# Performance work log

Measured on AMD Instinct MI355X. Metric: run time of the kernel, lower is better.

The kernel has to match this reference:

```python
import jax, jax.numpy as jnp
import numpy as np

N_NODES = 100_000
N_EDGES = 1_600_000
N_GRAPHS = 64
EPS = 1e-7  # GENConv message epsilon
D_IN, D_H, D_OUT, OUT_DIM = 128, 192, 128, 10


def _w(k, fan_in, fan_out):
    return jax.random.normal(k, (fan_in, fan_out), jnp.float32) * (1.0 / np.sqrt(fan_in))


def setup_inputs() -> dict:
    key = jax.random.key(0)
    ks = jax.random.split(key, 8)
    return {
        "x": jax.random.normal(ks[0], (N_NODES, D_IN), jnp.float32),
        "W0": _w(ks[1], D_IN, D_H), "b0": jnp.zeros((D_H,), jnp.float32),
        "W1": _w(ks[2], D_H, D_H), "b1": jnp.zeros((D_H,), jnp.float32),
        "W2": _w(ks[3], D_H, D_H), "b2": jnp.zeros((D_H,), jnp.float32),
        "W3": _w(ks[4], D_H, D_OUT), "b3": jnp.zeros((D_OUT,), jnp.float32),
        "Wfc": _w(ks[5], D_OUT, OUT_DIM), "bfc": jnp.zeros((OUT_DIM,), jnp.float32),
        "edge_index": jax.random.randint(ks[6], (2, N_EDGES), 0, N_NODES, jnp.int32),
        "batch": jnp.sort(jax.random.randint(ks[7], (N_NODES,), 0, N_GRAPHS, jnp.int32)),
    }


def _genconv(x, W, b, src, dst):
    # GENConv (num_layers=1, aggr='add'): message = relu(x_j) + eps,
    # scatter-add to dst, residual add, single Linear MLP.
    msg = jax.nn.relu(x[src]) + EPS          # [E, d]
    agg = jax.ops.segment_sum(msg, dst, num_segments=N_NODES)  # [N, d]
    return (x + agg) @ W + b


def reference(x, W0, b0, W1, b1, W2, b2, W3, b3, Wfc, bfc, edge_index, batch):
    src, dst = edge_index[0], edge_index[1]  # source_to_target flow
    for W, b in ((W0, b0), (W1, b1), (W2, b2), (W3, b3)):
        x = _genconv(x, W, b, src, dst)
    # global mean pool over graphs
    sums = jax.ops.segment_sum(x, batch, num_segments=N_GRAPHS)
    counts = jax.ops.segment_sum(jnp.ones((x.shape[0],), x.dtype), batch,
                                 num_segments=N_GRAPHS)
    pooled = sums / jnp.maximum(counts, 1.0)[:, None]  # [G, D_OUT]
    logits = pooled @ Wfc + bfc                        # [G, OUT_DIM]
    return jax.nn.log_softmax(logits, axis=1)
```

## Files before the change

kernel.cpp:

```cpp
#include <hip/hip_runtime.h>
#include <hip/hip_bf16.h>
#include <stdint.h>

constexpr int NN = 100000;
constexpr int NE = 1600000;
constexpr int NG = 64;
constexpr int S  = 192;
constexpr int NB_SCAN = 98;
constexpr int NN8 = 100352;
constexpr unsigned int ZOFF = (unsigned int)NN * 384u;

constexpr int PREP_INDEG_BLK = 1563;
constexpr int PREP_CONVX_BLK = 12500;
constexpr int PREP_CONVW_BLK = 384;
constexpr int PREP_GB_BLK    = 391;
constexpr int PREP_GRID = PREP_INDEG_BLK + PREP_CONVX_BLK + PREP_CONVW_BLK + PREP_GB_BLK;

constexpr int EG_BLOCKS = 391;
constexpr int HROW = 50048;
constexpr int SROW = HROW / 8;

typedef __bf16 bf16x8 __attribute__((ext_vector_type(8)));
typedef float  f32x16 __attribute__((ext_vector_type(16)));
typedef float  f32x2  __attribute__((ext_vector_type(2)));

union U16x4 { uint4 u; bf16x8 b; };

__device__ __forceinline__ float bl(unsigned int u) { return __uint_as_float(u << 16); }
__device__ __forceinline__ float bh(unsigned int u) { return __uint_as_float(u & 0xffff0000u); }
__device__ __forceinline__ float b16f(unsigned short u) { return __uint_as_float(((unsigned int)u) << 16); }
__device__ __forceinline__ unsigned int fb(float f) {
    unsigned int u = __float_as_uint(f);
    return (u + 0x7fffu + ((u >> 16) & 1u)) >> 16;
}
__device__ __forceinline__ unsigned int prelu(unsigned int u) {
    unsigned int r;
    asm("v_pk_max_f16 %0, %1, %2" : "=v"(r) : "v"(u), "v"(0u));
    return r;
}
__device__ __forceinline__ unsigned int cnt2bf(unsigned int h) {
    float f0 = (float)(h & 0xffffu);
    float f1 = (float)(h >> 16);
    return (__float_as_uint(f0) >> 16) | (__float_as_uint(f1) & 0xffff0000u);
}

__global__ __launch_bounds__(256) void k_prep(const float* __restrict__ x,
                                              const int* __restrict__ ei,
                                              const int* __restrict__ bat,
                                              const float* __restrict__ W0, const float* __restrict__ W1,
                                              const float* __restrict__ W2,
                                              unsigned short* __restrict__ A_,
                                              int* __restrict__ indeg8, int* __restrict__ slot,
                                              unsigned short* __restrict__ T0, unsigned short* __restrict__ T1,
                                              unsigned short* __restrict__ T2,
                                              int* __restrict__ nstart) {
    const int b = blockIdx.x;
    if (b < PREP_INDEG_BLK) {
        int e4 = (b * 256 + threadIdx.x) * 4;
        if (e4 < NE) {
            int* cp = indeg8 + (b & 7) * NN8;
            int4 d = *(const int4*)(ei + NE + e4);
            int4 sl;
            sl.x = atomicAdd(&cp[d.x], 1);
            sl.y = atomicAdd(&cp[d.y], 1);
            sl.z = atomicAdd(&cp[d.z], 1);
            sl.w = atomicAdd(&cp[d.w], 1);
            *(int4*)(slot + e4) = sl;
        }
    } else if (b < PREP_INDEG_BLK + PREP_CONVX_BLK) {
        int id = (b - PREP_INDEG_BLK) * 256 + threadIdx.x;
        if (id < 96) ((unsigned int*)(A_ + (size_t)NN * S))[id] = 0u;
        int row = id >> 5, c4 = id & 31;
        float4 v = ((const float4*)x)[id];
        uint2 a;
        a.x = fb(v.x) | (fb(v.y) << 16);
        a.y = fb(v.z) | (fb(v.w) << 16);
        *(uint2*)(A_ + row * S + c4 * 4) = a;
    } else if (b < PREP_INDEG_BLK + PREP_CONVX_BLK + PREP_CONVW_BLK) {
        int id = (b - PREP_INDEG_BLK - PREP_CONVX_BLK) * 256 + threadIdx.x;
        const float* W; unsigned short* T; int N, base;
        if      (id < 24576) { W = W0; T = T0; N = 192; base = 0;     }
        else if (id < 61440) { W = W1; T = T1; N = 192; base = 24576; }
        else                 { W = W2; T = T2; N = 192; base = 61440; }
        int lid = id - base;
        int ci = lid >> 3, j = lid & 7;
        int kc = ci / N, n = ci % N;
        T[lid] = (unsigned short)fb(W[(kc * 8 + j) * N + n]);
    } else {
        int n = (b - PREP_INDEG_BLK - PREP_CONVX_BLK - PREP_CONVW_BLK) * 256 + threadIdx.x;
        if (n < NN) {
            int b0 = bat[n];
            int bprev = (n == 0) ? -1 : bat[n - 1];
            for (int g = bprev + 1; g <= b0; g++) nstart[g] = n;
            if (n == NN - 1)
                for (int g = b0 + 1; g < NG; g++) nstart[g] = NN;
        }
    }
}

__global__ __launch_bounds__(1024) void k_scan1(const int* __restrict__ indeg8,
                                                int* __restrict__ indeg,
                                                unsigned short* __restrict__ pxcd,
                                                int* __restrict__ offs,
                                                int* __restrict__ partials,
                                                float* __restrict__ zero_region) {
    __shared__ int s[1024];
    int t = threadIdx.x;
    int gid = blockIdx.x * 1024 + t;
    int v = 0;
    if (gid < NN) {
        int run = 0;
#pragma unroll
        for (int x = 0; x < 8; x++) {
            int c = indeg8[x * NN8 + gid];
            pxcd[x * NN8 + gid] = (unsigned short)run;
            run += c;
        }
        v = run;
        indeg[gid] = run;
    }
    if (blockIdx.x == 0) {
        for (int i = t; i < 12416; i += 1024) zero_region[i] = 0.f;
    }
    s[t] = v;
    __syncthreads();
    for (int d = 1; d < 1024; d <<= 1) {
        int tv = (t >= d) ? s[t - d] : 0;
        __syncthreads();
        s[t] += tv;
        __syncthreads();
    }
    if (gid < NN) offs[gid + 1] = s[t];
    if (t == 1023) partials[blockIdx.x] = s[1023];
}

__device__ __forceinline__ int toff(const int* __restrict__ offs, const int* __restrict__ part, int j) {
    return j ? (offs[j] + part[(j - 1) >> 10]) : 0;
}

__global__ __launch_bounds__(256) void k_fill(const int* __restrict__ ei, const int* __restrict__ offs,
                                              const int* __restrict__ praw,
                                              const int* __restrict__ slot,
                                              const unsigned short* __restrict__ pxcd,
                                              int* __restrict__ csr,
                                              int* __restrict__ part2) {
    __shared__ int s[128];
    __shared__ int spx[128];
    const int t = threadIdx.x;
    int v = 0;
    if (t < 128) {
        v = (t < NB_SCAN) ? praw[t] : 0;
        s[t] = v;
    }
    __syncthreads();
    for (int d = 1; d < 128; d <<= 1) {
        int tv = (t < 128 && t >= d) ? s[t - d] : 0;
        __syncthreads();
        if (t < 128) s[t] += tv;
        __syncthreads();
    }
    if (t < 128) spx[t] = s[t] - v;
    __syncthreads();
    if (blockIdx.x == 0 && t < NB_SCAN) part2[t] = spx[t];

    int e4 = (blockIdx.x * 256 + t) * 4;
    if (e4 >= NE) return;
    const unsigned short* px = pxcd + (size_t)((e4 >> 10) & 7) * NN8;
    int4 sv = *(const int4*)(ei + e4);
    int4 dv = *(const int4*)(ei + NE + e4);
    int4 sl = *(const int4*)(slot + e4);
    csr[(dv.x ? offs[dv.x] + spx[(dv.x - 1) >> 10] : 0) + px[dv.x] + sl.x] = sv.x;
    csr[(dv.y ? offs[dv.y] + spx[(dv.y - 1) >> 10] : 0) + px[dv.y] + sl.y] = sv.y;
    csr[(dv.z ? offs[dv.z] + spx[(dv.z - 1) >> 10] : 0) + px[dv.z] + sl.z] = sv.z;
    csr[(dv.w ? offs[dv.w] + spx[(dv.w - 1) >> 10] : 0) + px[dv.w] + sl.w] = sv.w;
}

__global__ __launch_bounds__(256, 8) void k_agg192(const unsigned short* __restrict__ Ain,
                                                   unsigned short* __restrict__ Yout,
                                                   const int* __restrict__ offs,
                                                   const int* __restrict__ part,
                                                   const int* __restrict__ indeg,
                                                   const int* __restrict__ csr) {
    const int w = threadIdx.x >> 6, lane = threadIdx.x & 63;
    const int i = __builtin_amdgcn_readfirstlane(blockIdx.x * 4 + w);
    const bool act = lane < 48;
    const int deg   = __builtin_amdgcn_readfirstlane(indeg[i]);
    const int start = __builtin_amdgcn_readfirstlane(toff(offs, part, i));
    const int fo = (act ? lane : 47) * 8;
    const char* Ab = (const char*)Ain;

    f32x2 A01, A23;
    {
        uint2 p = *(const uint2*)(Ab + (size_t)i * 384 + fo);
        const float ed = 1e-7f * (float)deg;
        A01 = (f32x2){bl(p.x) + ed, bh(p.x) + ed};
        A23 = (f32x2){bl(p.y) + ed, bh(p.y) + ed};
    }

    const int* ecsr = csr + start;
    for (int e = 0; e < deg; e += 16) {
        unsigned int off[16];
#pragma unroll
        for (int k = 0; k < 16; k++) {
            int v = ecsr[e + k];
            off[k] = (e + k < deg) ? (unsigned int)v * 384u : ZOFF;
        }
        uint2 p[16];
#pragma unroll
        for (int k = 0; k < 16; k++)
            p[k] = *(const uint2*)(Ab + (size_t)off[k] + fo);
#pragma unroll
        for (int k = 0; k < 16; k++) {
            unsigned int rx = prelu(p[k].x), ry = prelu(p[k].y);
            A01 += (f32x2){bl(rx), bh(rx)};
            A23 += (f32x2){bl(ry), bh(ry)};
        }
    }
    if (act) {
        uint2 o;
        o.x = fb(A01.x) | (fb(A01.y) << 16);
        o.y = fb(A23.x) | (fb(A23.y) << 16);
        *(uint2*)(Yout + (size_t)i * S + lane * 4) = o;
    }
}

__global__ __launch_bounds__(256, 8) void k_agg128(const unsigned short* __restrict__ Ain,
                                                   unsigned short* __restrict__ Yout,
                                                   const int* __restrict__ offs,
                                                   const int* __restrict__ part,
                                                   const int* __restrict__ indeg,
                                                   const int* __restrict__ csr) {
    const int w = threadIdx.x >> 6, lane = threadIdx.x & 63;
    const int i = __builtin_amdgcn_readfirstlane(blockIdx.x * 4 + w);
    const int deg   = __builtin_amdgcn_readfirstlane(indeg[i]);
    const int start = __builtin_amdgcn_readfirstlane(toff(offs, part, i));
    const int fo = lane * 4;
    const char* Ab = (const char*)Ain;

    f32x2 A01;
    {
        unsigned int p = *(const unsigned int*)(Ab + (size_t)i * 384 + fo);
        const float ed = 1e-7f * (float)deg;
        A01 = (f32x2){bl(p) + ed, bh(p) + ed};
    }

    const int* ecsr = csr + start;
    for (int e = 0; e < deg; e += 16) {
        unsigned int off[16];
#pragma unroll
        for (int k = 0; k < 16; k++) {
            int v = ecsr[e + k];
            off[k] = (e + k < deg) ? (unsigned int)v * 384u : ZOFF;
        }
        unsigned int q[16];
#pragma unroll
        for (int k = 0; k < 16; k++)
            q[k] = *(const unsigned int*)(Ab + (size_t)off[k] + fo);
#pragma unroll
        for (int k = 0; k < 16; k++) {
            unsigned int r = prelu(q[k]);
            A01 += (f32x2){bl(r), bh(r)};
        }
    }
    *(unsigned int*)(Yout + (size_t)i * S + lane * 2) =
        fb(A01.x) | (fb(A01.y) << 16);
}

template <int K, int N>
__global__ __launch_bounds__(256) void k_gemm(const unsigned short* __restrict__ Yin,
                                              const unsigned short* __restrict__ WtC,
                                              const float* __restrict__ bias,
                                              unsigned short* __restrict__ Aout) {
    static_assert(K % 16 == 0 && N % 32 == 0, "");
    const int w = threadIdx.x >> 6, lane = threadIdx.x & 63;
    const int rt = blockIdx.x * 4 + w;
    if (rt >= (NN / 32)) return;
    const int hl = lane >> 5, lr = lane & 31;
    const int row0 = rt * 32;
    f32x16 acc[N / 32];
#pragma unroll
    for (int c = 0; c < N / 32; c++)
#pragma unroll
        for (int r = 0; r < 16; r++) acc[c][r] = 0.f;

    const unsigned short* ap = Yin + (row0 + lr) * S + hl * 8;
    const uint4* b4 = (const uint4*)WtC;
#pragma unroll
    for (int ks = 0; ks < K / 16; ks++) {
        U16x4 a;
        a.u = *(const uint4*)(ap + ks * 16);
#pragma unroll
        for (int c = 0; c < N / 32; c++) {
            U16x4 b;
            b.u = b4[(ks * 2 + hl) * N + c * 32 + lr];
            acc[c] = __builtin_amdgcn_mfma_f32_32x32x16_bf16(a.b, b.b, acc[c], 0, 0, 0);
        }
    }
#pragma unroll
    for (int c = 0; c < N / 32; c++) {
        const int col = c * 32 + lr;
        const float bc = bias[col];
#pragma unroll
        for (int r = 0; r < 16; r++) {
            const int row = row0 + (r & 3) + 8 * (r >> 2) + 4 * hl;
            Aout[row * S + col] = (unsigned short)fb(acc[c][r] + bc);
        }
    }
}

__global__ __launch_bounds__(256) void k_histpool(const int* __restrict__ csr,
                                                  const int* __restrict__ offs,
                                                  const int* __restrict__ part,
                                                  const int* __restrict__ nstart,
                                                  unsigned int* __restrict__ hist,
                                                  const unsigned short* __restrict__ X3,
                                                  const int* __restrict__ bat,
                                                  const int* __restrict__ indeg,
                                                  float* __restrict__ sums, float* __restrict__ cnt,
                                                  float* __restrict__ degsum) {
    __shared__ unsigned int hlds[SROW];
    const int b = blockIdx.x;
    if (b < 512) {
        const int g = b >> 3, q = b & 7;
        const unsigned int q0 = (unsigned int)(q * SROW);
        for (int i = threadIdx.x; i < SROW; i += 256) hlds[i] = 0u;
        __syncthreads();
        const int s0 = toff(offs, part, nstart[g]);
        const int s1 = (g == NG - 1) ? NE : toff(offs, part, nstart[g + 1]);
        for (int p = s0 + threadIdx.x; p < s1; p += 256) {
            int src = csr[p];
            unsigned int h = (unsigned int)src >> 1;
            if (h - q0 < (unsigned int)SROW)
                atomicAdd(&hlds[h - q0], 1u << (16 * (src & 1)));
        }
        __syncthreads();
        unsigned int* hrow = hist + (size_t)g * HROW + q0;
        for (int i = threadIdx.x; i < SROW; i += 256) hrow[i] = hlds[i];
    } else {
        const int pb = b - 512;
        const int f = threadIdx.x;
        if (f >= 192) return;
        int n0 = pb * 50;
        int n1 = min(n0 + 50, NN);
        int cur = bat[n0];
        float acc = 0.f;
        int run = 0, dacc = 0;
        for (int n = n0; n < n1; n++) {
            int g = bat[n];
            if (g != cur) {
                atomicAdd(&sums[cur * 192 + f], acc);
                if (f == 0) { atomicAdd(&cnt[cur], (float)run); atomicAdd(&degsum[cur], (float)dacc); }
                acc = 0.f; run = 0; dacc = 0; cur = g;
            }
            acc += b16f(X3[(size_t)n * S + f]);
            run++;
            if (f == 0) dacc += indeg[n];
        }
        atomicAdd(&sums[cur * 192 + f], acc);
        if (f == 0) { atomicAdd(&cnt[cur], (float)run); atomicAdd(&degsum[cur], (float)dacc); }
    }
}

__global__ __launch_bounds__(384) void k_egemm(const unsigned short* __restrict__ X3,
                                               const unsigned int* __restrict__ hist,
                                               float* __restrict__ partials) {
    const int wv = threadIdx.x >> 6, lane = threadIdx.x & 63;
    const int b = blockIdx.x;
    const int j0 = b * 256;
    const int hl = lane >> 5, lr = lane & 31;
    const int feat = wv * 32 + lr;
    f32x16 acc[2];
#pragma unroll
    for (int m = 0; m < 2; m++)
#pragma unroll
        for (int r = 0; r < 16; r++) acc[m][r] = 0.f;

    for (int kk = 0; kk < 16; kk++) {
        const int jh = (j0 >> 1) + kk * 8 + hl * 4;
        U16x4 af[2];
#pragma unroll
        for (int m = 0; m < 2; m++) {
            uint4 h = *(const uint4*)(hist + (size_t)(m * 32 + lr) * HROW + jh);
            af[m].u = (uint4){cnt2bf(h.x), cnt2bf(h.y), cnt2bf(h.z), cnt2bf(h.w)};
        }
        U16x4 bf;
#pragma unroll
        for (int tp = 0; tp < 4; tp++) {
            int je = j0 + kk * 16 + hl * 8 + tp * 2;
            int ja = min(je, NN), jb = min(je + 1, NN);
            unsigned int u0 = X3[(size_t)ja * S + feat];
            unsigned int u1 = X3[(size_t)jb * S + feat];
            ((unsigned int*)&bf.u)[tp] = prelu(u0 | (u1 << 16));
        }
#pragma unroll
        for (int m = 0; m < 2; m++)
            acc[m] = __builtin_amdgcn_mfma_f32_32x32x16_bf16(af[m].b, bf.b, acc[m], 0, 0, 0);
    }
    float* pb = partials + (size_t)b * 12288;
#pragma unroll
    for (int m = 0; m < 2; m++)
#pragma unroll
        for (int r = 0; r < 16; r++) {
            const int g = m * 32 + (r & 3) + 8 * (r >> 2) + 4 * hl;
            pb[g * 192 + feat] = acc[m][r];
        }
}

__global__ __launch_bounds__(192) void k_head(const float* __restrict__ sums,
                                              const float* __restrict__ partials,
                                              const float* __restrict__ cnt, const float* __restrict__ degsum,
                                              const float* __restrict__ W3, const float* __restrict__ b3,
                                              const float* __restrict__ Wfc, const float* __restrict__ bfc,
                                              float* __restrict__ out) {
    __shared__ float py[192];
    __shared__ float tl[128];
    __shared__ float lg[10];
    const int g = blockIdx.x, t = threadIdx.x;
    const float inv = 1.f / fmaxf(cnt[g], 1.f);
    const float ed = 1e-7f * degsum[g];
    const float* pp = partials + g * 192 + t;
    float s0 = 0.f, s1 = 0.f, s2 = 0.f, s3 = 0.f;
    int p = 0;
    for (; p + 4 <= 391; p += 4) {
        s0 += pp[(size_t)(p + 0) * 12288];
        s1 += pp[(size_t)(p + 1) * 12288];
        s2 += pp[(size_t)(p + 2) * 12288];
        s3 += pp[(size_t)(p + 3) * 12288];
    }
    for (; p < 391; p++) s0 += pp[(size_t)p * 12288];
    py[t] = (sums[g * 192 + t] + ((s0 + s1) + (s2 + s3)) + ed) * inv;
    __syncthreads();
    if (t < 128) {
        float tf = b3[t];
        for (int k = 0; k < 192; k++) tf += py[k] * W3[k * 128 + t];
        tl[t] = tf;
    }
    __syncthreads();
    if (t < 10) {
        float sf = bfc[t];
        for (int f = 0; f < 128; f++) sf += tl[f] * Wfc[f * 10 + t];
        lg[t] = sf;
    }
    __syncthreads();
    if (t < 10) {
        float m = lg[0];
        for (int k = 1; k < 10; k++) m = fmaxf(m, lg[k]);
        float se = 0.f;
        for (int k = 0; k < 10; k++) se += expf(lg[k] - m);
        out[g * 10 + t] = lg[t] - m - logf(se);
    }
}

constexpr size_t A0_OFF      = 0;
constexpr size_t A1_OFF      = 38400384;
constexpr size_t SLOT_REL    = 0;
constexpr size_t INDEG8_REL  = 6400000;
constexpr size_t PXCD_REL    = 9611264;
constexpr size_t HIST_REL    = 0;
constexpr size_t PARTS_REL   = 12812288;
constexpr size_t CSR_OFF     = 76800768;
constexpr size_t OFFS_OFF    = 83200768;
constexpr size_t INDEG_OFF   = 83600896;
constexpr size_t SUMS_OFF    = 84000896;
constexpr size_t CNT_OFF     = 84050048;
constexpr size_t DEGS_OFF    = 84050304;
constexpr size_t PART_OFF    = 84050560;
constexpr size_t PART2_OFF   = 84051072;
constexpr size_t NSTART_OFF  = 84051584;
constexpr size_t WT0_OFF     = 84051840;
constexpr size_t WT1_OFF     = 84100992;
constexpr size_t WT2_OFF     = 84174720;

extern "C" void kernel_launch(void* const* d_in, const int* in_sizes, int n_in,
                              void* d_out, int out_size, void* d_ws, size_t ws_size,
                              hipStream_t stream) {
    const float* x   = (const float*)d_in[0];
    const float* W0  = (const float*)d_in[1];
    const float* b0  = (const float*)d_in[2];
    const float* W1  = (const float*)d_in[3];
    const float* b1  = (const float*)d_in[4];
    const float* W2  = (const float*)d_in[5];
    const float* b2  = (const float*)d_in[6];
    const float* W3  = (const float*)d_in[7];
    const float* b3  = (const float*)d_in[8];
    const float* Wfc = (const float*)d_in[9];
    const float* bfc = (const float*)d_in[10];
    const int*   ei  = (const int*)d_in[11];
    const int*   bat = (const int*)d_in[12];
    float* out = (float*)d_out;

    char* ws = (char*)d_ws;
    unsigned short* A0  = (unsigned short*)(ws + A0_OFF);
    unsigned short* A1  = (unsigned short*)(ws + A1_OFF);
    int* slot            = (int*)(ws + A1_OFF + SLOT_REL);
    int* indeg8          = (int*)(ws + A1_OFF + INDEG8_REL);
    unsigned short* pxcd = (unsigned short*)(ws + A1_OFF + PXCD_REL);
    unsigned int* hist   = (unsigned int*)(ws + A1_OFF + HIST_REL);
    float* parts         = (float*)(ws + A1_OFF + PARTS_REL);
    int* csr    = (int*)(ws + CSR_OFF);
    int* offs   = (int*)(ws + OFFS_OFF);
    int* indeg  = (int*)(ws + INDEG_OFF);
    int* part   = (int*)(ws + PART_OFF);
    int* part2  = (int*)(ws + PART2_OFF);
    int* nstart = (int*)(ws + NSTART_OFF);
    unsigned short* Wt0 = (unsigned short*)(ws + WT0_OFF);
    unsigned short* Wt1 = (unsigned short*)(ws + WT1_OFF);
    unsigned short* Wt2 = (unsigned short*)(ws + WT2_OFF);
    float* sums   = (float*)(ws + SUMS_OFF);
    float* cnt    = (float*)(ws + CNT_OFF);
    float* degsum = (float*)(ws + DEGS_OFF);

    hipMemsetAsync(ws + A1_OFF + INDEG8_REL, 0, 3211264, stream);

    k_prep<<<PREP_GRID, 256, 0, stream>>>(x, ei, bat, W0, W1, W2, A0, indeg8, slot,
                                          Wt0, Wt1, Wt2, nstart);

    k_scan1<<<NB_SCAN, 1024, 0, stream>>>(indeg8, indeg, pxcd, offs, part, sums);
    k_fill<<<(NE / 4 + 255) / 256, 256, 0, stream>>>(ei, offs, part, slot, pxcd, csr, part2);

    const int AGG_GRID  = NN / 4;
    const int GEMM_GRID = (NN / 32 + 3) / 4;

    k_agg128<<<AGG_GRID, 256, 0, stream>>>(A0, A1, offs, part2, indeg, csr);
    k_gemm<128, 192><<<GEMM_GRID, 256, 0, stream>>>(A1, Wt0, b0, A0);
    k_agg192<<<AGG_GRID, 256, 0, stream>>>(A0, A1, offs, part2, indeg, csr);
    k_gemm<192, 192><<<GEMM_GRID, 256, 0, stream>>>(A1, Wt1, b1, A0);
    k_agg192<<<AGG_GRID, 256, 0, stream>>>(A0, A1, offs, part2, indeg, csr);
    k_gemm<192, 192><<<GEMM_GRID, 256, 0, stream>>>(A1, Wt2, b2, A0);

    k_histpool<<<2512, 256, 0, stream>>>(csr, offs, part2, nstart, hist, A0, bat, indeg,
                                         sums, cnt, degsum);
    k_egemm<<<EG_BLOCKS, 384, 0, stream>>>(A0, hist, parts);
    k_head<<<NG, 192, 0, stream>>>(sums, parts, cnt, degsum, W3, b3, Wfc, bfc, out);
}
```

Measured before the change: 609.2 us.

## Fold histogram into first aggregation launch and merge pooling into egemm

```diff
diff --git a/kernel.cpp b/kernel.cpp
--- a/kernel.cpp
+++ b/kernel.cpp
@@ -18,7 +18,9 @@
 
 constexpr int EG_BLOCKS = 391;
 constexpr int HROW = 50048;
-constexpr int SROW = HROW / 8;
+constexpr int SROW = HROW / 16;
+constexpr int HIST_BLOCKS = NG * 16;
+constexpr int POOL_BLOCKS = 2000;
 
 typedef __bf16 bf16x8 __attribute__((ext_vector_type(8)));
 typedef float  f32x16 __attribute__((ext_vector_type(16)));
@@ -175,6 +177,89 @@
     csr[(dv.w ? offs[dv.w] + spx[(dv.w - 1) >> 10] : 0) + px[dv.w] + sl.w] = sv.w;
 }
 
+__device__ __forceinline__ void hist_block(int hb, const int* __restrict__ csr,
+                                           const int* __restrict__ offs,
+                                           const int* __restrict__ part,
+                                           const int* __restrict__ nstart,
+                                           unsigned int* __restrict__ hist,
+                                           unsigned int* __restrict__ hlds) {
+    const int g = hb >> 4, q = hb & 15;
+    const unsigned int q0 = (unsigned int)(q * SROW);
+    for (int i = threadIdx.x; i < SROW; i += 256) hlds[i] = 0u;
+    __syncthreads();
+    const int s0 = toff(offs, part, nstart[g]);
+    const int s1 = (g == NG - 1) ? NE : toff(offs, part, nstart[g + 1]);
+    for (int p = s0 + threadIdx.x; p < s1; p += 256) {
+        int src = csr[p];
+        unsigned int h = (unsigned int)src >> 1;
+        if (h - q0 < (unsigned int)SROW)
+            atomicAdd(&hlds[h - q0], 1u << (16 * (src & 1)));
+    }
+    __syncthreads();
+    unsigned int* hrow = hist + (size_t)g * HROW + q0;
+    for (int i = threadIdx.x; i < SROW; i += 256) hrow[i] = hlds[i];
+}
+
+__global__ __launch_bounds__(256, 8) void k_agg128(const unsigned short* __restrict__ Ain,
+                                                   unsigned short* __restrict__ Yout,
+                                                   const int* __restrict__ offs,
+                                                   const int* __restrict__ part,
+                                                   const int* __restrict__ indeg,
+                                                   const int* __restrict__ csr,
+                                                   const int* __restrict__ nstart,
+                                                   unsigned int* __restrict__ hist,
+                                                   int histBlocks) {
+    __shared__ unsigned int hlds[SROW];
+    if (blockIdx.x < (unsigned)histBlocks) {
+        hist_block(blockIdx.x, csr, offs, part, nstart, hist, hlds);
+        return;
+    }
+    const int vb = blockIdx.x - histBlocks;
+    const int w = threadIdx.x >> 6, lane = threadIdx.x & 63;
+    const int i = __builtin_amdgcn_readfirstlane(vb * 4 + w);
+    const int deg   = __builtin_amdgcn_readfirstlane(indeg[i]);
+    const int start = __builtin_amdgcn_readfirstlane(toff(offs, part, i));
+    const int fo = lane * 4;
+    const char* Ab = (const char*)Ain;
+
+    f32x2 A01;
+    {
+        unsigned int p = *(const unsigned int*)(Ab + (size_t)i * 384 + fo);
+        const float ed = 1e-7f * (float)deg;
+        A01 = (f32x2){bl(p) + ed, bh(p) + ed};
+    }
+
+    const int* ecsr = csr + start;
+    for (int e = 0; e < deg; e += 16) {
+        unsigned int off[16];
+#pragma unroll
+        for (int k = 0; k < 16; k++) {
+            int v = ecsr[e + k];
+            off[k] = (e + k < deg) ? (unsigned int)v * 384u : ZOFF;
+        }
+        unsigned int q[16];
+#pragma unroll
+        for (int k = 0; k < 16; k++)
+            q[k] = *(const unsigned int*)(Ab + (size_t)off[k] + fo);
+#pragma unroll
+        for (int k = 0; k < 16; k++) {
+            unsigned int r = prelu(q[k]);
+            A01 += (f32x2){bl(r), bh(r)};
+        }
+    }
+    *(unsigned int*)(Yout + (size_t)i * S + lane * 2) =
+        fb(A01.x) | (fb(A01.y) << 16);
+}
+
+__global__ __launch_bounds__(256) void k_histsolo(const int* __restrict__ csr,
+                                                  const int* __restrict__ offs,
+                                                  const int* __restrict__ part,
+                                                  const int* __restrict__ nstart,
+                                                  unsigned int* __restrict__ hist) {
+    __shared__ unsigned int hlds[SROW];
+    hist_block(blockIdx.x, csr, offs, part, nstart, hist, hlds);
+}
+
 __global__ __launch_bounds__(256, 8) void k_agg192(const unsigned short* __restrict__ Ain,
                                                    unsigned short* __restrict__ Yout,
                                                    const int* __restrict__ offs,
@@ -224,48 +309,6 @@
     }
 }
 
-__global__ __launch_bounds__(256, 8) void k_agg128(const unsigned short* __restrict__ Ain,
-                                                   unsigned short* __restrict__ Yout,
-                                                   const int* __restrict__ offs,
-                                                   const int* __restrict__ part,
-                                                   const int* __restrict__ indeg,
-                                                   const int* __restrict__ csr) {
-    const int w = threadIdx.x >> 6, lane = threadIdx.x & 63;
-    const int i = __builtin_amdgcn_readfirstlane(blockIdx.x * 4 + w);
-    const int deg   = __builtin_amdgcn_readfirstlane(indeg[i]);
-    const int start = __builtin_amdgcn_readfirstlane(toff(offs, part, i));
-    const int fo = lane * 4;
-    const char* Ab = (const char*)Ain;
-
-    f32x2 A01;
-    {
-        unsigned int p = *(const unsigned int*)(Ab + (size_t)i * 384 + fo);
-        const float ed = 1e-7f * (float)deg;
-        A01 = (f32x2){bl(p) + ed, bh(p) + ed};
-    }
-
-    const int* ecsr = csr + start;
-    for (int e = 0; e < deg; e += 16) {
-        unsigned int off[16];
-#pragma unroll
-        for (int k = 0; k < 16; k++) {
-            int v = ecsr[e + k];
-            off[k] = (e + k < deg) ? (unsigned int)v * 384u : ZOFF;
-        }
-        unsigned int q[16];
-#pragma unroll
-        for (int k = 0; k < 16; k++)
-            q[k] = *(const unsigned int*)(Ab + (size_t)off[k] + fo);
-#pragma unroll
-        for (int k = 0; k < 16; k++) {
-            unsigned int r = prelu(q[k]);
-            A01 += (f32x2){bl(r), bh(r)};
-        }
-    }
-    *(unsigned int*)(Yout + (size_t)i * S + lane * 2) =
-        fb(A01.x) | (fb(A01.y) << 16);
-}
-
 template <int K, int N>
 __global__ __launch_bounds__(256) void k_gemm(const unsigned short* __restrict__ Yin,
                                               const unsigned short* __restrict__ WtC,
@@ -308,36 +351,15 @@
     }
 }
 
-__global__ __launch_bounds__(256) void k_histpool(const int* __restrict__ csr,
-                                                  const int* __restrict__ offs,
-                                                  const int* __restrict__ part,
-                                                  const int* __restrict__ nstart,
-                                                  unsigned int* __restrict__ hist,
-                                                  const unsigned short* __restrict__ X3,
-                                                  const int* __restrict__ bat,
-                                                  const int* __restrict__ indeg,
-                                                  float* __restrict__ sums, float* __restrict__ cnt,
-                                                  float* __restrict__ degsum) {
-    __shared__ unsigned int hlds[SROW];
-    const int b = blockIdx.x;
-    if (b < 512) {
-        const int g = b >> 3, q = b & 7;
-        const unsigned int q0 = (unsigned int)(q * SROW);
-        for (int i = threadIdx.x; i < SROW; i += 256) hlds[i] = 0u;
-        __syncthreads();
-        const int s0 = toff(offs, part, nstart[g]);
-        const int s1 = (g == NG - 1) ? NE : toff(offs, part, nstart[g + 1]);
-        for (int p = s0 + threadIdx.x; p < s1; p += 256) {
-            int src = csr[p];
-            unsigned int h = (unsigned int)src >> 1;
-            if (h - q0 < (unsigned int)SROW)
-                atomicAdd(&hlds[h - q0], 1u << (16 * (src & 1)));
-        }
-        __syncthreads();
-        unsigned int* hrow = hist + (size_t)g * HROW + q0;
-        for (int i = threadIdx.x; i < SROW; i += 256) hrow[i] = hlds[i];
-    } else {
-        const int pb = b - 512;
+__global__ __launch_bounds__(384) void k_egemm(const unsigned short* __restrict__ X3,
+                                               const unsigned int* __restrict__ hist,
+                                               float* __restrict__ partials,
+                                               const int* __restrict__ bat,
+                                               const int* __restrict__ indeg,
+                                               float* __restrict__ sums, float* __restrict__ cnt,
+                                               float* __restrict__ degsum) {
+    if (blockIdx.x < POOL_BLOCKS) {
+        const int pb = blockIdx.x;
         const int f = threadIdx.x;
         if (f >= 192) return;
         int n0 = pb * 50;
@@ -358,14 +380,10 @@
         }
         atomicAdd(&sums[cur * 192 + f], acc);
         if (f == 0) { atomicAdd(&cnt[cur], (float)run); atomicAdd(&degsum[cur], (float)dacc); }
-    }
-}
-
-__global__ __launch_bounds__(384) void k_egemm(const unsigned short* __restrict__ X3,
-                                               const unsigned int* __restrict__ hist,
-                                               float* __restrict__ partials) {
+        return;
+    }
+    const int b = blockIdx.x - POOL_BLOCKS;
     const int wv = threadIdx.x >> 6, lane = threadIdx.x & 63;
-    const int b = blockIdx.x;
     const int j0 = b * 256;
     const int hl = lane >> 5, lr = lane & 31;
     const int feat = wv * 32 + lr;
@@ -421,13 +439,13 @@
     const float* pp = partials + g * 192 + t;
     float s0 = 0.f, s1 = 0.f, s2 = 0.f, s3 = 0.f;
     int p = 0;
-    for (; p + 4 <= 391; p += 4) {
+    for (; p + 4 <= EG_BLOCKS; p += 4) {
         s0 += pp[(size_t)(p + 0) * 12288];
         s1 += pp[(size_t)(p + 1) * 12288];
         s2 += pp[(size_t)(p + 2) * 12288];
         s3 += pp[(size_t)(p + 3) * 12288];
     }
-    for (; p < 391; p++) s0 += pp[(size_t)p * 12288];
+    for (; p < EG_BLOCKS; p++) s0 += pp[(size_t)p * 12288];
     py[t] = (sums[g * 192 + t] + ((s0 + s1) + (s2 + s3)) + ed) * inv;
     __syncthreads();
     if (t < 128) {
@@ -470,6 +488,8 @@
 constexpr size_t WT0_OFF     = 84051840;
 constexpr size_t WT1_OFF     = 84100992;
 constexpr size_t WT2_OFF     = 84174720;
+constexpr size_t HIST2_OFF   = 84248576;
+constexpr size_t WS_NEED_BIG = 97060864;
 
 extern "C" void kernel_launch(void* const* d_in, const int* in_sizes, int n_in,
                               void* d_out, int out_size, void* d_ws, size_t ws_size,
@@ -495,7 +515,6 @@
     int* slot            = (int*)(ws + A1_OFF + SLOT_REL);
     int* indeg8          = (int*)(ws + A1_OFF + INDEG8_REL);
     unsigned short* pxcd = (unsigned short*)(ws + A1_OFF + PXCD_REL);
-    unsigned int* hist   = (unsigned int*)(ws + A1_OFF + HIST_REL);
     float* parts         = (float*)(ws + A1_OFF + PARTS_REL);
     int* csr    = (int*)(ws + CSR_OFF);
     int* offs   = (int*)(ws + OFFS_OFF);
@@ -510,6 +529,9 @@
     float* cnt    = (float*)(ws + CNT_OFF);
     float* degsum = (float*)(ws + DEGS_OFF);
 
+    const bool big = ws_size >= WS_NEED_BIG;
+    unsigned int* hist = (unsigned int*)(big ? (ws + HIST2_OFF) : (ws + A1_OFF + HIST_REL));
+
     hipMemsetAsync(ws + A1_OFF + INDEG8_REL, 0, 3211264, stream);
 
     k_prep<<<PREP_GRID, 256, 0, stream>>>(x, ei, bat, W0, W1, W2, A0, indeg8, slot,
@@ -520,16 +542,20 @@
 
     const int AGG_GRID  = NN / 4;
     const int GEMM_GRID = (NN / 32 + 3) / 4;
-
-    k_agg128<<<AGG_GRID, 256, 0, stream>>>(A0, A1, offs, part2, indeg, csr);
+    const int hb = big ? HIST_BLOCKS : 0;
+
+    k_agg128<<<AGG_GRID + hb, 256, 0, stream>>>(A0, A1, offs, part2, indeg, csr,
+                                                nstart, hist, hb);
     k_gemm<128, 192><<<GEMM_GRID, 256, 0, stream>>>(A1, Wt0, b0, A0);
     k_agg192<<<AGG_GRID, 256, 0, stream>>>(A0, A1, offs, part2, indeg, csr);
     k_gemm<192, 192><<<GEMM_GRID, 256, 0, stream>>>(A1, Wt1, b1, A0);
     k_agg192<<<AGG_GRID, 256, 0, stream>>>(A0, A1, offs, part2, indeg, csr);
     k_gemm<192, 192><<<GEMM_GRID, 256, 0, stream>>>(A1, Wt2, b2, A0);
 
-    k_histpool<<<2512, 256, 0, stream>>>(csr, offs, part2, nstart, hist, A0, bat, indeg,
-                                         sums, cnt, degsum);
-    k_egemm<<<EG_BLOCKS, 384, 0, stream>>>(A0, hist, parts);
+    if (!big)
+        k_histsolo<<<HIST_BLOCKS, 256, 0, stream>>>(csr, offs, part2, nstart, hist);
+
+    k_egemm<<<POOL_BLOCKS + EG_BLOCKS, 384, 0, stream>>>(A0, hist, parts, bat, indeg,
+                                                         sums, cnt, degsum);
     k_head<<<NG, 192, 0, stream>>>(sums, parts, cnt, degsum, W3, b3, Wfc, bfc, out);
 }
```

Measured after the change: 609.5 us. No clear change (+0.1%).
